# Performance work log

Hardware: AMD Instinct MI355X
Metric: run time of the kernel (lower is better)

## Reference

```python
import jax, jax.numpy as jnp
import numpy as np

N_NODES = 50000
N_EDGES = 1600000
IN_DIM = 512
HID = 128  # conv1 out = 2*HID = 256, conv2 out = HID = 128
EPS = 1e-5


def gcn_conv(x, src, dst, W, b, n_nodes):
    """PyG GCNConv: x' = D^{-1/2} (A + I) D^{-1/2} (x W) + b (self loops added)."""
    h = x @ W  # [N, out]
    loop = jnp.arange(n_nodes, dtype=src.dtype)
    s = jnp.concatenate([src, loop])  # sources incl. self loops
    d = jnp.concatenate([dst, loop])  # targets incl. self loops
    ones = jnp.ones(s.shape[0], dtype=h.dtype)
    deg = jax.ops.segment_sum(ones, d, num_segments=n_nodes)  # in-degree on targets
    dis = jnp.where(deg > 0, jax.lax.rsqrt(jnp.maximum(deg, 1.0)), 0.0)
    norm = dis[s] * dis[d]  # [E+N]
    msg = norm[:, None] * h[s]  # gather + scale, [E+N, out]
    out = jax.ops.segment_sum(msg, d, num_segments=n_nodes)  # scatter-add
    return out + b


def batch_norm(x, gamma, beta):
    """BatchNorm1d with batch statistics (biased variance), eps=1e-5."""
    mean = jnp.mean(x, axis=0)
    var = jnp.mean(jnp.square(x - mean), axis=0)
    return (x - mean) * jax.lax.rsqrt(var + EPS) * gamma + beta


def setup_inputs() -> dict:
    key = jax.random.key(0)
    ks = jax.random.split(key, 8)
    x = jax.random.normal(ks[0], (N_NODES, IN_DIM), dtype=jnp.float32)
    edge_index = jax.random.randint(ks[1], (2, N_EDGES), 0, N_NODES, dtype=jnp.int64)
    d1 = 2 * HID
    W1 = jax.random.normal(ks[2], (IN_DIM, d1), dtype=jnp.float32) / np.sqrt(IN_DIM)
    b1 = jnp.zeros((d1,), dtype=jnp.float32)
    gamma1 = jnp.ones((d1,), dtype=jnp.float32)
    beta1 = jnp.zeros((d1,), dtype=jnp.float32)
    W2 = jax.random.normal(ks[3], (d1, HID), dtype=jnp.float32) / np.sqrt(d1)
    b2 = jnp.zeros((HID,), dtype=jnp.float32)
    gamma2 = jnp.ones((HID,), dtype=jnp.float32)
    beta2 = jnp.zeros((HID,), dtype=jnp.float32)
    return {"x": x, "edge_index": edge_index, "W1": W1, "b1": b1,
            "gamma1": gamma1, "beta1": beta1, "W2": W2, "b2": b2,
            "gamma2": gamma2, "beta2": beta2}


def reference(x, edge_index, W1, b1, gamma1, beta1, W2, b2, gamma2, beta2):
    src, dst = edge_index[0], edge_index[1]
    h = gcn_conv(x, src, dst, W1, b1, N_NODES)
    h = batch_norm(h, gamma1, beta1)
    h = jax.nn.relu(h)
    # dropout: identity in eval mode (deterministic reference)
    h = gcn_conv(h, src, dst, W2, b2, N_NODES)
    h = batch_norm(h, gamma2, beta2)
    return h
```

## Files before the change

### kernel.cpp

```cpp
#include <hip/hip_runtime.h>
#include <hip/hip_bf16.h>


#define NN 50000
#define NE 1600000
#define DIN 512
#define D1 256
#define D2 128
#define EPSV 1e-5f
#define NBUCK 16
#define BSZ 3125
#define NDB 128
#define NPB 391
#define CAP 16384

typedef __attribute__((ext_vector_type(8))) short bf16x8_t;
typedef __attribute__((ext_vector_type(4))) float f32x4_t;

__device__ __forceinline__ float bf2f(unsigned short u) {
  return __uint_as_float(((unsigned int)u) << 16);
}
__device__ __forceinline__ unsigned short f2bf(float f) {
  unsigned int u = __float_as_uint(f);
  u += 0x7fffu + ((u >> 16) & 1u);
  return (unsigned short)(u >> 16);
}
__device__ __forceinline__ unsigned int pk2(float a, float b) {
  __hip_bfloat162 h = __float22bfloat162_rn(make_float2(a, b));
  union { __hip_bfloat162 h; unsigned int u; } c;
  c.h = h;
  return c.u;
}

__global__ void k_zero(int* __restrict__ gcursor, float* __restrict__ stats) {
  int i = blockIdx.x * 256 + threadIdx.x;
  if (i < NDB) gcursor[i] = 0;
  if (i < (D1 * 2 + D2 * 2)) stats[i] = 0.0f;
}

__global__ __launch_bounds__(256) void k_part(const int* __restrict__ src,
                                              const int* __restrict__ dst,
                                              int* __restrict__ gcursor,
                                              unsigned int* __restrict__ part) {
  __shared__ int hist[NDB];
  __shared__ int curs[NDB];
  const int t = threadIdx.x;
  const int EB = NE / 256;
  const int e0 = blockIdx.x * EB;
  if (t < NDB) hist[t] = 0;
  __syncthreads();
  for (int i = t; i < EB; i += 256) {
    int d = dst[e0 + i];
    atomicAdd(&hist[d / NPB], 1);
  }
  __syncthreads();
  if (t < NDB) {
    int c = hist[t];
    curs[t] = (c > 0) ? atomicAdd(&gcursor[t], c) : 0;
  }
  __syncthreads();
  for (int i = t; i < EB; i += 256) {
    int s = src[e0 + i];
    int d = dst[e0 + i];
    int b = d / NPB;
    int dl = d - b * NPB;
    int sb = (unsigned)s / BSZ;
    unsigned int w = (unsigned)s | ((unsigned)dl << 16) | ((unsigned)sb << 25);
    int pos = atomicAdd(&curs[b], 1);
    if (pos < CAP) part[(size_t)b * CAP + pos] = w;
  }
}

__global__ void k_bscan(const int* __restrict__ gcursor, int* __restrict__ ebase) {
  __shared__ int s[NDB];
  int t = threadIdx.x;
  int v = gcursor[t];
  s[t] = v;
  __syncthreads();
  for (int off = 1; off < NDB; off <<= 1) {
    int a = (t >= off) ? s[t - off] : 0;
    __syncthreads();
    s[t] += a;
    __syncthreads();
  }
  ebase[t] = s[t] - v;
  if (t == NDB - 1) ebase[NDB] = s[t];
}

__global__ __launch_bounds__(256) void k_build(const unsigned int* __restrict__ part,
                                               const int* __restrict__ gcursor,
                                               const int* __restrict__ ebase,
                                               int* __restrict__ row_ptr,
                                               float* __restrict__ dis,
                                               int* __restrict__ col) {
  const int NC = NPB * NBUCK;
  __shared__ int cnt[NC];
  __shared__ int tsum[256];
  const int b = blockIdx.x, t = threadIdx.x;
  int m = gcursor[b];
  if (m > CAP) m = CAP;
  const int base = ebase[b];
  const unsigned int* my = part + (size_t)b * CAP;
  for (int i = t; i < NC; i += 256) cnt[i] = 0;
  __syncthreads();
  for (int i = t; i < m; i += 256) {
    unsigned int w = my[i];
    atomicAdd(&cnt[((w >> 16) & 0x1ff) * NBUCK + (w >> 25)], 1);
  }
  __syncthreads();
  const int CHK = (NC + 255) / 256;
  int i0 = t * CHK;
  int sum = 0;
  for (int i = 0; i < CHK; i++) {
    int idx = i0 + i;
    if (idx < NC) sum += cnt[idx];
  }
  tsum[t] = sum;
  __syncthreads();
  for (int off = 1; off < 256; off <<= 1) {
    int a = (t >= off) ? tsum[t - off] : 0;
    __syncthreads();
    tsum[t] += a;
    __syncthreads();
  }
  int run = tsum[t] - sum;
  for (int i = 0; i < CHK; i++) {
    int idx = i0 + i;
    if (idx < NC) {
      int c = cnt[idx];
      cnt[idx] = run;
      run += c;
    }
  }
  __syncthreads();
  const int n0 = b * NPB;
  for (int dl = t; dl < NPB; dl += 256) {
    int n = n0 + dl;
    if (n < NN) {
      int st = cnt[dl * NBUCK];
      int en = (dl * NBUCK + NBUCK < NC) ? cnt[dl * NBUCK + NBUCK] : m;
      row_ptr[n] = base + st;
      dis[n] = rsqrtf((float)(en - st + 1));
    }
  }
  if (b == NDB - 1 && t == 0) row_ptr[NN] = base + m;
  __syncthreads();
  for (int i = t; i < m; i += 256) {
    unsigned int w = my[i];
    int pos = atomicAdd(&cnt[((w >> 16) & 0x1ff) * NBUCK + (w >> 25)], 1);
    col[base + pos] = w & 0xffff;
  }
}

__global__ void k_prep_w(const float* __restrict__ W1, const float* __restrict__ W2,
                         unsigned short* __restrict__ W1t, unsigned short* __restrict__ W2t) {
  int i = blockIdx.x * 256 + threadIdx.x;
  if (i < DIN * D1) {
    int n = i / DIN, k = i - n * DIN;
    W1t[i] = f2bf(W1[(size_t)k * D1 + n]);
  } else {
    int j = i - DIN * D1;
    int n = j / D1, k = j - n * D1;
    W2t[j] = f2bf(W2[(size_t)k * D2 + n]);
  }
}

__global__ __launch_bounds__(256) void k_gemm1(const float* __restrict__ A,
                                               const unsigned short* __restrict__ Bt,
                                               unsigned short* __restrict__ C, int M) {
  __shared__ unsigned short As[64 * 64];
  __shared__ unsigned short Bs[256 * 64];
  const int t = threadIdx.x;
  const int wave = t >> 6, lane = t & 63;
  const int m0 = blockIdx.x * 64;
  const int wn = wave * 64;
  const int l8 = lane >> 3;
  const int lbs = (lane & 7) ^ l8;
  const int row_c = lane & 15, quad = lane >> 4;

  f32x4_t acc[4][4];
#pragma unroll
  for (int i = 0; i < 4; i++)
#pragma unroll
    for (int j = 0; j < 4; j++) acc[i][j] = (f32x4_t){0.f, 0.f, 0.f, 0.f};

  for (int k0 = 0; k0 < DIN; k0 += 64) {
#pragma unroll
    for (int j = 0; j < 8; j++) {
      int chunk = wave * 8 + j;
      int row = chunk * 8 + l8;
      const unsigned short* g = Bt + (size_t)row * DIN + k0 + lbs * 8;
      __builtin_amdgcn_global_load_lds(
          (const __attribute__((address_space(1))) unsigned int*)g,
          (__attribute__((address_space(3))) unsigned int*)(Bs + chunk * 512), 16, 0, 0);
    }
#pragma unroll
    for (int i = 0; i < 2; i++) {
      int bid = i * 256 + t;
      int row = bid >> 3, pb = bid & 7;
      int lb = pb ^ (row & 7);
      int gm = m0 + row;
      if (gm >= M) gm = M - 1;
      const float4* s = (const float4*)(A + (size_t)gm * DIN + k0 + lb * 8);
      float4 v0 = s[0], v1 = s[1];
      uint4 o;
      o.x = pk2(v0.x, v0.y);
      o.y = pk2(v0.z, v0.w);
      o.z = pk2(v1.x, v1.y);
      o.w = pk2(v1.z, v1.w);
      *(uint4*)(As + row * 64 + pb * 8) = o;
    }
    __syncthreads();
#pragma unroll
    for (int ki = 0; ki < 2; ki++) {
      bf16x8_t af[4], bfr[4];
      int kb = ki * 4 + quad;
#pragma unroll
      for (int i = 0; i < 4; i++) {
        int ar = i * 16 + row_c;
        af[i] = *(const bf16x8_t*)(As + ar * 64 + ((kb ^ (ar & 7)) * 8));
        int br = wn + i * 16 + row_c;
        bfr[i] = *(const bf16x8_t*)(Bs + br * 64 + ((kb ^ (br & 7)) * 8));
      }
#pragma unroll
      for (int i = 0; i < 4; i++)
#pragma unroll
        for (int j = 0; j < 4; j++)
          acc[i][j] = __builtin_amdgcn_mfma_f32_16x16x32_bf16(af[i], bfr[j], acc[i][j], 0, 0, 0);
    }
    __syncthreads();
  }
#pragma unroll
  for (int i = 0; i < 4; i++) {
#pragma unroll
    for (int j = 0; j < 4; j++) {
      int colv = wn + j * 16 + row_c;
#pragma unroll
      for (int r = 0; r < 4; r++) {
        int gm = m0 + i * 16 + quad * 4 + r;
        if (gm < M) C[(size_t)gm * D1 + colv] = f2bf(acc[i][j][r]);
      }
    }
  }
}

__global__ void k_finalize1(const float* __restrict__ stats, const float* __restrict__ gamma,
                            const float* __restrict__ beta, float* __restrict__ sc1,
                            float* __restrict__ sh1) {
  int c = threadIdx.x;
  float mean = stats[c] * (1.0f / NN);
  float var = stats[D1 + c] * (1.0f / NN) - mean * mean;
  float sc = gamma[c] * rsqrtf(var + EPSV);
  sc1[c] = sc;
  sh1[c] = beta[c] - mean * sc;
}

__global__ __launch_bounds__(128) void k_gemm2(const unsigned short* __restrict__ A,
                                               const float* __restrict__ sc1,
                                               const float* __restrict__ sh1,
                                               const unsigned short* __restrict__ Bt,
                                               unsigned short* __restrict__ C, int M) {
  __shared__ unsigned short As[64 * 64];
  __shared__ unsigned short Bs[128 * 64];
  const int t = threadIdx.x;
  const int wave = t >> 6, lane = t & 63;
  const int m0 = blockIdx.x * 64;
  const int wn = wave * 64;
  const int l8 = lane >> 3;
  const int lbs = (lane & 7) ^ l8;
  const int row_c = lane & 15, quad = lane >> 4;

  f32x4_t acc[4][4];
#pragma unroll
  for (int i = 0; i < 4; i++)
#pragma unroll
    for (int j = 0; j < 4; j++) acc[i][j] = (f32x4_t){0.f, 0.f, 0.f, 0.f};

  for (int k0 = 0; k0 < D1; k0 += 64) {
#pragma unroll
    for (int j = 0; j < 8; j++) {
      int chunk = wave * 8 + j;
      int row = chunk * 8 + l8;
      const unsigned short* g = Bt + (size_t)row * D1 + k0 + lbs * 8;
      __builtin_amdgcn_global_load_lds(
          (const __attribute__((address_space(1))) unsigned int*)g,
          (__attribute__((address_space(3))) unsigned int*)(Bs + chunk * 512), 16, 0, 0);
    }
#pragma unroll
    for (int i = 0; i < 4; i++) {
      int bid = i * 128 + t;
      int row = bid >> 3, pb = bid & 7;
      int lb = pb ^ (row & 7);
      int gm = m0 + row;
      if (gm >= M) gm = M - 1;
      int colb = k0 + lb * 8;
      uint4 raw = *(const uint4*)(A + (size_t)gm * D1 + colb);
      float4 scA = *(const float4*)(sc1 + colb);
      float4 scB = *(const float4*)(sc1 + colb + 4);
      float4 shA = *(const float4*)(sh1 + colb);
      float4 shB = *(const float4*)(sh1 + colb + 4);
      float f0 = fmaxf(fmaf(bf2f((unsigned short)(raw.x & 0xffff)), scA.x, shA.x), 0.f);
      float f1 = fmaxf(fmaf(bf2f((unsigned short)(raw.x >> 16)),    scA.y, shA.y), 0.f);
      float f2 = fmaxf(fmaf(bf2f((unsigned short)(raw.y & 0xffff)), scA.z, shA.z), 0.f);
      float f3 = fmaxf(fmaf(bf2f((unsigned short)(raw.y >> 16)),    scA.w, shA.w), 0.f);
      float f4 = fmaxf(fmaf(bf2f((unsigned short)(raw.z & 0xffff)), scB.x, shB.x), 0.f);
      float f5 = fmaxf(fmaf(bf2f((unsigned short)(raw.z >> 16)),    scB.y, shB.y), 0.f);
      float f6 = fmaxf(fmaf(bf2f((unsigned short)(raw.w & 0xffff)), scB.z, shB.z), 0.f);
      float f7 = fmaxf(fmaf(bf2f((unsigned short)(raw.w >> 16)),    scB.w, shB.w), 0.f);
      uint4 o;
      o.x = pk2(f0, f1);
      o.y = pk2(f2, f3);
      o.z = pk2(f4, f5);
      o.w = pk2(f6, f7);
      *(uint4*)(As + row * 64 + pb * 8) = o;
    }
    __syncthreads();
#pragma unroll
    for (int ki = 0; ki < 2; ki++) {
      bf16x8_t af[4], bfr[4];
      int kb = ki * 4 + quad;
#pragma unroll
      for (int i = 0; i < 4; i++) {
        int ar = i * 16 + row_c;
        af[i] = *(const bf16x8_t*)(As + ar * 64 + ((kb ^ (ar & 7)) * 8));
        int br = wn + i * 16 + row_c;
        bfr[i] = *(const bf16x8_t*)(Bs + br * 64 + ((kb ^ (br & 7)) * 8));
      }
#pragma unroll
      for (int i = 0; i < 4; i++)
#pragma unroll
        for (int j = 0; j < 4; j++)
          acc[i][j] = __builtin_amdgcn_mfma_f32_16x16x32_bf16(af[i], bfr[j], acc[i][j], 0, 0, 0);
    }
    __syncthreads();
  }
#pragma unroll
  for (int i = 0; i < 4; i++) {
#pragma unroll
    for (int j = 0; j < 4; j++) {
      int colv = wn + j * 16 + row_c;
#pragma unroll
      for (int r = 0; r < 4; r++) {
        int gm = m0 + i * 16 + quad * 4 + r;
        if (gm < M) C[(size_t)gm * D2 + colv] = f2bf(acc[i][j][r]);
      }
    }
  }
}

__global__ __launch_bounds__(256) void k_agg1(const unsigned short* __restrict__ H,
                                              const int* __restrict__ row_ptr,
                                              const int* __restrict__ col,
                                              const float* __restrict__ dis,
                                              const float* __restrict__ bias,
                                              unsigned short* __restrict__ OUT) {
  int n = blockIdx.x * 4 + (threadIdx.x >> 6);
  int lane = threadIdx.x & 63;
  if (n >= NN) return;
  float dn = dis[n];
  ushort4 v = ((const ushort4*)(H + (size_t)n * D1))[lane];
  float wsf = dn * dn;
  float a0 = wsf * bf2f(v.x), a1 = wsf * bf2f(v.y);
  float a2 = wsf * bf2f(v.z), a3 = wsf * bf2f(v.w);
  int e = row_ptr[n], e1 = row_ptr[n + 1];
  while (e < e1) {
    int cnt = e1 - e;
    if (cnt > 64) cnt = 64;
    int li = (lane < cnt) ? lane : (cnt - 1);
    int cv = col[e + li];
    float dwv = dis[cv] * dn;
    int dwu = __float_as_int(dwv);
    int b = 0;
    for (; b + 8 <= cnt; b += 8) {
      int s[8];
      float w[8];
      ushort4 u[8];
#pragma unroll
      for (int k = 0; k < 8; k++) {
        s[k] = __builtin_amdgcn_readlane(cv, b + k);
        w[k] = __int_as_float(__builtin_amdgcn_readlane(dwu, b + k));
      }
#pragma unroll
      for (int k = 0; k < 8; k++)
        u[k] = ((const ushort4*)(H + (size_t)s[k] * D1))[lane];
#pragma unroll
      for (int k = 0; k < 8; k++) {
        a0 += w[k] * bf2f(u[k].x);
        a1 += w[k] * bf2f(u[k].y);
        a2 += w[k] * bf2f(u[k].z);
        a3 += w[k] * bf2f(u[k].w);
      }
    }
    for (; b < cnt; b++) {
      int sK = __builtin_amdgcn_readlane(cv, b);
      float wK = __int_as_float(__builtin_amdgcn_readlane(dwu, b));
      ushort4 uK = ((const ushort4*)(H + (size_t)sK * D1))[lane];
      a0 += wK * bf2f(uK.x);
      a1 += wK * bf2f(uK.y);
      a2 += wK * bf2f(uK.z);
      a3 += wK * bf2f(uK.w);
    }
    e += cnt;
  }
  int c = lane * 4;
  a0 += bias[c]; a1 += bias[c + 1]; a2 += bias[c + 2]; a3 += bias[c + 3];
  ushort4 o;
  o.x = f2bf(a0); o.y = f2bf(a1); o.z = f2bf(a2); o.w = f2bf(a3);
  ((ushort4*)(OUT + (size_t)n * D1))[lane] = o;
}

__global__ __launch_bounds__(256) void k_agg2(const unsigned short* __restrict__ H,
                                              const int* __restrict__ row_ptr,
                                              const int* __restrict__ col,
                                              const float* __restrict__ dis,
                                              const float* __restrict__ bias,
                                              float* __restrict__ OUT) {
  int n = blockIdx.x * 4 + (threadIdx.x >> 6);
  int lane = threadIdx.x & 63;
  if (n >= NN) return;
  float dn = dis[n];
  ushort2 v = ((const ushort2*)(H + (size_t)n * D2))[lane];
  float wsf = dn * dn;
  float a0 = wsf * bf2f(v.x), a1 = wsf * bf2f(v.y);
  int e = row_ptr[n], e1 = row_ptr[n + 1];
  while (e < e1) {
    int cnt = e1 - e;
    if (cnt > 64) cnt = 64;
    int li = (lane < cnt) ? lane : (cnt - 1);
    int cv = col[e + li];
    float dwv = dis[cv] * dn;
    int dwu = __float_as_int(dwv);
    int b = 0;
    for (; b + 8 <= cnt; b += 8) {
      int s[8];
      float w[8];
      ushort2 u[8];
#pragma unroll
      for (int k = 0; k < 8; k++) {
        s[k] = __builtin_amdgcn_readlane(cv, b + k);
        w[k] = __int_as_float(__builtin_amdgcn_readlane(dwu, b + k));
      }
#pragma unroll
      for (int k = 0; k < 8; k++)
        u[k] = ((const ushort2*)(H + (size_t)s[k] * D2))[lane];
#pragma unroll
      for (int k = 0; k < 8; k++) {
        a0 += w[k] * bf2f(u[k].x);
        a1 += w[k] * bf2f(u[k].y);
      }
    }
    for (; b < cnt; b++) {
      int sK = __builtin_amdgcn_readlane(cv, b);
      float wK = __int_as_float(__builtin_amdgcn_readlane(dwu, b));
      ushort2 uK = ((const ushort2*)(H + (size_t)sK * D2))[lane];
      a0 += wK * bf2f(uK.x);
      a1 += wK * bf2f(uK.y);
    }
    e += cnt;
  }
  int c = lane * 2;
  a0 += bias[c]; a1 += bias[c + 1];
  ((float2*)(OUT + (size_t)n * D2))[lane] = make_float2(a0, a1);
}

__global__ void k_stats1(const unsigned short* __restrict__ X, float* __restrict__ stats) {
  int t = threadIdx.x;
  int r0 = blockIdx.x * 64;
  int r1 = (r0 + 64 < NN) ? r0 + 64 : NN;
  float s = 0.f, q = 0.f;
  for (int r = r0; r < r1; r++) {
    float v = bf2f(X[(size_t)r * D1 + t]);
    s += v;
    q += v * v;
  }
  atomicAdd(&stats[t], s);
  atomicAdd(&stats[D1 + t], q);
}

__global__ void k_stats2(const float* __restrict__ X, float* __restrict__ stats) {
  int t = threadIdx.x;
  int r0 = blockIdx.x * 128;
  int r1 = (r0 + 128 < NN) ? r0 + 128 : NN;
  float s = 0.f, q = 0.f;
  for (int r = r0; r < r1; r++) {
    float v = X[(size_t)r * D2 + t];
    s += v;
    q += v * v;
  }
  atomicAdd(&stats[t], s);
  atomicAdd(&stats[D2 + t], q);
}

__global__ void k_apply2(float* __restrict__ X, const float* __restrict__ stats,
                         const float* __restrict__ gamma, const float* __restrict__ beta) {
  int i = blockIdx.x * blockDim.x + threadIdx.x;
  int c = i & (D2 - 1);
  float mean = stats[c] * (1.0f / NN);
  float var = stats[D2 + c] * (1.0f / NN) - mean * mean;
  float sc = gamma[c] * rsqrtf(var + EPSV);
  X[i] = (X[i] - mean) * sc + beta[c];
}

extern "C" void kernel_launch(void* const* d_in, const int* in_sizes, int n_in,
                              void* d_out, int out_size, void* d_ws, size_t ws_size,
                              hipStream_t stream) {
  const float* x  = (const float*)d_in[0];
  const int* ei   = (const int*)d_in[1];
  const int* srcv = ei;
  const int* dstv = ei + NE;
  const float* W1  = (const float*)d_in[2];
  const float* b1  = (const float*)d_in[3];
  const float* g1  = (const float*)d_in[4];
  const float* be1 = (const float*)d_in[5];
  const float* W2  = (const float*)d_in[6];
  const float* b2  = (const float*)d_in[7];
  const float* g2  = (const float*)d_in[8];
  const float* be2 = (const float*)d_in[9];
  float* out = (float*)d_out;

  char* ws = (char*)d_ws;
  size_t off = 0;
  auto alloc = [&](size_t bytes) {
    size_t cur = off;
    off = (off + bytes + 255) & ~(size_t)255;
    return cur;
  };
  int* row_ptr   = (int*)(ws + alloc((NN + 1) * 4));
  float* dis     = (float*)(ws + alloc(NN * 4));
  int* gcursor   = (int*)(ws + alloc(NDB * 4));
  int* ebase     = (int*)(ws + alloc((NDB + 1) * 4));
  float* stats   = (float*)(ws + alloc((D1 * 2 + D2 * 2) * 4));
  float* sc1     = (float*)(ws + alloc(D1 * 4));
  float* sh1     = (float*)(ws + alloc(D1 * 4));
  int* col       = (int*)(ws + alloc((size_t)NE * 4));
  unsigned short* H1  = (unsigned short*)(ws + alloc((size_t)NN * D1 * 2));
  unsigned short* A1  = (unsigned short*)(ws + alloc((size_t)NN * D1 * 2));
  unsigned short* H2  = (unsigned short*)(ws + alloc((size_t)NN * D2 * 2));
  unsigned short* W1t = (unsigned short*)(ws + alloc((size_t)DIN * D1 * 2));
  unsigned short* W2t = (unsigned short*)(ws + alloc((size_t)D1 * D2 * 2));
  float* stats2 = stats + D1 * 2;
  unsigned int* part = (unsigned int*)H1;

  k_zero<<<3, 256, 0, stream>>>(gcursor, stats);
  k_part<<<256, 256, 0, stream>>>(srcv, dstv, gcursor, part);
  k_bscan<<<1, NDB, 0, stream>>>(gcursor, ebase);
  k_build<<<NDB, 256, 0, stream>>>(part, gcursor, ebase, row_ptr, dis, col);

  k_prep_w<<<(DIN * D1 + D1 * D2) / 256, 256, 0, stream>>>(W1, W2, W1t, W2t);

  const int mb = (NN + 63) / 64;

  k_gemm1<<<mb, 256, 0, stream>>>(x, W1t, H1, NN);
  k_agg1<<<(NN + 3) / 4, 256, 0, stream>>>(H1, row_ptr, col, dis, b1, A1);
  k_stats1<<<(NN + 63) / 64, 256, 0, stream>>>(A1, stats);
  k_finalize1<<<1, 256, 0, stream>>>(stats, g1, be1, sc1, sh1);

  k_gemm2<<<mb, 128, 0, stream>>>(A1, sc1, sh1, W2t, H2, NN);
  k_agg2<<<(NN + 3) / 4, 256, 0, stream>>>(H2, row_ptr, col, dis, b2, out);
  k_stats2<<<(NN + 127) / 128, 128, 0, stream>>>(out, stats2);
  k_apply2<<<NN * D2 / 256, 256, 0, stream>>>(out, stats2, g2, be2);
}
```

Baseline: 516.1 us.

## Split layer-1 aggregation into two feature-half passes for cache locality

The layer-1 neighbor aggregation now runs as two launches, each gathering only half of the 256 bf16 features, 128 columns at a time. The random-access working set per pass is halved (about 12.8MB instead of 25.6MB of H1 rows), so gathered rows are more likely to hit L2 or the infinity cache. The cost is reading the CSR indices and degree scales twice, doubling wave count with half-width 4-byte loads per lane, and an extra kernel launch.

```diff
diff --git a/kernel.cpp b/kernel.cpp
--- a/kernel.cpp
+++ b/kernel.cpp
@@ -348,20 +348,21 @@
   }
 }
 
-__global__ __launch_bounds__(256) void k_agg1(const unsigned short* __restrict__ H,
-                                              const int* __restrict__ row_ptr,
-                                              const int* __restrict__ col,
-                                              const float* __restrict__ dis,
-                                              const float* __restrict__ bias,
-                                              unsigned short* __restrict__ OUT) {
+__global__ __launch_bounds__(256) void k_agg1h(const unsigned short* __restrict__ H,
+                                               const int* __restrict__ row_ptr,
+                                               const int* __restrict__ col,
+                                               const float* __restrict__ dis,
+                                               const float* __restrict__ bias,
+                                               unsigned short* __restrict__ OUT,
+                                               int half) {
   int n = blockIdx.x * 4 + (threadIdx.x >> 6);
   int lane = threadIdx.x & 63;
   if (n >= NN) return;
+  const unsigned short* Hh = H + half * 128;
   float dn = dis[n];
-  ushort4 v = ((const ushort4*)(H + (size_t)n * D1))[lane];
+  ushort2 v = ((const ushort2*)(Hh + (size_t)n * D1))[lane];
   float wsf = dn * dn;
   float a0 = wsf * bf2f(v.x), a1 = wsf * bf2f(v.y);
-  float a2 = wsf * bf2f(v.z), a3 = wsf * bf2f(v.w);
   int e = row_ptr[n], e1 = row_ptr[n + 1];
   while (e < e1) {
     int cnt = e1 - e;
@@ -374,7 +375,7 @@
     for (; b + 8 <= cnt; b += 8) {
       int s[8];
       float w[8];
-      ushort4 u[8];
+      ushort2 u[8];
 #pragma unroll
       for (int k = 0; k < 8; k++) {
         s[k] = __builtin_amdgcn_readlane(cv, b + k);
@@ -382,31 +383,27 @@
       }
 #pragma unroll
       for (int k = 0; k < 8; k++)
-        u[k] = ((const ushort4*)(H + (size_t)s[k] * D1))[lane];
+        u[k] = ((const ushort2*)(Hh + (size_t)s[k] * D1))[lane];
 #pragma unroll
       for (int k = 0; k < 8; k++) {
         a0 += w[k] * bf2f(u[k].x);
         a1 += w[k] * bf2f(u[k].y);
-        a2 += w[k] * bf2f(u[k].z);
-        a3 += w[k] * bf2f(u[k].w);
       }
     }
     for (; b < cnt; b++) {
       int sK = __builtin_amdgcn_readlane(cv, b);
       float wK = __int_as_float(__builtin_amdgcn_readlane(dwu, b));
-      ushort4 uK = ((const ushort4*)(H + (size_t)sK * D1))[lane];
+      ushort2 uK = ((const ushort2*)(Hh + (size_t)sK * D1))[lane];
       a0 += wK * bf2f(uK.x);
       a1 += wK * bf2f(uK.y);
-      a2 += wK * bf2f(uK.z);
-      a3 += wK * bf2f(uK.w);
     }
     e += cnt;
   }
-  int c = lane * 4;
-  a0 += bias[c]; a1 += bias[c + 1]; a2 += bias[c + 2]; a3 += bias[c + 3];
-  ushort4 o;
-  o.x = f2bf(a0); o.y = f2bf(a1); o.z = f2bf(a2); o.w = f2bf(a3);
-  ((ushort4*)(OUT + (size_t)n * D1))[lane] = o;
+  int c = half * 128 + lane * 2;
+  a0 += bias[c]; a1 += bias[c + 1];
+  ushort2 o;
+  o.x = f2bf(a0); o.y = f2bf(a1);
+  ((ushort2*)(OUT + (size_t)n * D1 + half * 128))[lane] = o;
 }
 
 __global__ __launch_bounds__(256) void k_agg2(const unsigned short* __restrict__ H,
@@ -551,7 +548,8 @@
   const int mb = (NN + 63) / 64;
 
   k_gemm1<<<mb, 256, 0, stream>>>(x, W1t, H1, NN);
-  k_agg1<<<(NN + 3) / 4, 256, 0, stream>>>(H1, row_ptr, col, dis, b1, A1);
+  k_agg1h<<<(NN + 3) / 4, 256, 0, stream>>>(H1, row_ptr, col, dis, b1, A1, 0);
+  k_agg1h<<<(NN + 3) / 4, 256, 0, stream>>>(H1, row_ptr, col, dis, b1, A1, 1);
   k_stats1<<<(NN + 63) / 64, 256, 0, stream>>>(A1, stats);
   k_finalize1<<<1, 256, 0, stream>>>(stats, g1, be1, sc1, sh1);
 
```

Result: no change. 512.7 us (-0.7%).
